# Optimization experiments

Measured on AMD Instinct MI355X. Metric: run time of the kernel, lower is better.

The kernel has to match this reference:

```python
import jax, jax.numpy as jnp
import numpy as np

K = 5
EPS = 1e-08


def setup_inputs() -> dict:
    key = jax.random.key(0)
    x = jax.random.normal(key, (8192, 512), dtype=jnp.float32)
    return {"x": x}


def reference(x):
    n = x.shape[0]
    # torch: everything below through topk is under no_grad, and x is rebound
    # to the normalized tensor, so the whole graph is detached from the input.
    xn = x / jnp.linalg.norm(x, axis=1, keepdims=True)
    xn = jax.lax.stop_gradient(xn)
    dots = xn @ xn.T                                  # [N, N]
    dots = jnp.where(jnp.eye(n, dtype=bool), jnp.float32(-1.0), dots)
    _, topk_idx = jax.lax.top_k(dots, K)              # [N, K]
    x_neighbors = xn[topk_idx]                        # [N, K, D]
    diffs = xn[:, None, :] - x_neighbors              # [N, K, D]
    distances = jnp.linalg.norm(diffs, axis=-1)       # [N, K]
    mean_rho = distances.mean(axis=1)                 # [N]
    loss = -jnp.mean(jnp.log(mean_rho + EPS))
    return loss
```

## Files before the change

kernel.cpp:

```cpp
#include <hip/hip_runtime.h>
#include <math.h>

#define NROWS 8192
#define DIM   512
#define KNN   5
#define EPSV  1e-8f

#define BM 128
#define BN 128
#define BK 32
#define NT (NROWS / BM)
#define NT64 (NROWS / 64)
#define NKS (DIM / BK)
#define NWORK 2080
#define NSEL (NROWS / 4)

typedef __attribute__((ext_vector_type(8))) _Float16 f16x8;
typedef __attribute__((ext_vector_type(4))) float    f32x4;

__device__ __forceinline__ void gload16(const _Float16* g, _Float16* l) {
    __builtin_amdgcn_global_load_lds(
        (const __attribute__((address_space(1))) void*)g,
        (__attribute__((address_space(3))) void*)l, 16, 0, 0);
}

__device__ __forceinline__ void cmpswap(float& a, float& b) {
    const float hi = fmaxf(a, b), lo = fminf(a, b);
    a = hi; b = lo;
}

__device__ __forceinline__ void merge5(float a[KNN], const float b[KNN]) {
    const float c0 = fmaxf(a[0], b[0]);
    const float c1 = fmaxf(fmaxf(a[1], b[1]), fminf(a[0], b[0]));
    const float c2 = fmaxf(fmaxf(a[2], b[2]),
                           fmaxf(fminf(a[0], b[1]), fminf(a[1], b[0])));
    const float c3 = fmaxf(fmaxf(a[3], b[3]),
                           fmaxf(fminf(a[0], b[2]),
                                 fmaxf(fminf(a[1], b[1]), fminf(a[2], b[0]))));
    const float c4 = fmaxf(fmaxf(a[4], b[4]),
                           fmaxf(fmaxf(fminf(a[0], b[3]), fminf(a[1], b[2])),
                                 fmaxf(fminf(a[2], b[1]), fminf(a[3], b[0]))));
    a[0] = c0; a[1] = c1; a[2] = c2; a[3] = c3; a[4] = c4;
}

__global__ __launch_bounds__(256) void norm_kernel(const float* __restrict__ x,
                                                   _Float16* __restrict__ xnh) {
    const int wv = threadIdx.x >> 6, lane = threadIdx.x & 63;
    const int row = blockIdx.x * 4 + wv;
    const float4* xr = (const float4*)(x + (size_t)row * DIM) + lane * 2;
    const float4 a = xr[0];
    const float4 b = xr[1];
    float s = a.x * a.x + a.y * a.y + a.z * a.z + a.w * a.w
            + b.x * b.x + b.y * b.y + b.z * b.z + b.w * b.w;
    #pragma unroll
    for (int off = 1; off < 64; off <<= 1) s += __shfl_xor(s, off, 64);
    const float inv = 1.0f / sqrtf(s);
    const f16x8 h = { (_Float16)(a.x * inv), (_Float16)(a.y * inv),
                      (_Float16)(a.z * inv), (_Float16)(a.w * inv),
                      (_Float16)(b.x * inv), (_Float16)(b.y * inv),
                      (_Float16)(b.z * inv), (_Float16)(b.w * inv) };
    *(f16x8*)(xnh + (size_t)row * DIM + lane * 8) = h;
}

__global__ __launch_bounds__(256) void dots_top3_kernel(const _Float16* __restrict__ xnh,
                                                        float* __restrict__ M3) {
    int I, J;
    {
        int rem = (int)(blockIdx.x & 7) * (NWORK / 8) + (int)(blockIdx.x >> 3);
        int found = 0;
        for (int SI = 0; SI < 8 && !found; ++SI) {
            for (int SJ = SI; SJ < 8 && !found; ++SJ) {
                const int sz = (SI == SJ) ? 36 : 64;
                if (rem < sz) {
                    if (SI == SJ) {
                        int i = 0, r2 = rem;
                        while (r2 >= 8 - i) { r2 -= 8 - i; ++i; }
                        I = SI * 8 + i;
                        J = SJ * 8 + i + r2;
                    } else {
                        I = SI * 8 + (rem >> 3);
                        J = SJ * 8 + (rem & 7);
                    }
                    found = 1;
                } else {
                    rem -= sz;
                }
            }
        }
    }

    __shared__ __align__(16) _Float16 As[BM * BK];
    __shared__ __align__(16) _Float16 Bs[BN * BK];

    const int tid    = threadIdx.x;
    const int lane   = tid & 63;
    const int wv     = tid >> 6;
    const int wm     = wv >> 1;
    const int wn     = wv & 1;
    const int m_lane = lane & 15;
    const int quad   = lane >> 4;

    const int i0 = I * BM;
    const int j0 = J * BN;

    const int rowlocal = (m_lane >> 2) * 16 + quad * 4 + (m_lane & 3);
    const int myrow    = i0 + wm * 64 + rowlocal;

    const int rchunk = (quad ^ ((m_lane >> 1) & 3)) * 8;

    f32x4 acc[4][4];
    #pragma unroll
    for (int m = 0; m < 4; ++m)
        #pragma unroll
        for (int n = 0; n < 4; ++n)
            acc[m][n] = (f32x4){0.f, 0.f, 0.f, 0.f};

    for (int ks = 0; ks < NKS; ++ks) {
        const int k0 = ks * BK;
        #pragma unroll
        for (int q = 0; q < 2; ++q) {
            const int s  = tid + q * 256;
            const int r  = s >> 2;
            const int kg = (s & 3) ^ ((s >> 3) & 3);
            gload16(xnh + (size_t)(i0 + r) * DIM + k0 + kg * 8, As + s * 8);
            gload16(xnh + (size_t)(j0 + r) * DIM + k0 + kg * 8, Bs + s * 8);
        }
        __syncthreads();

        f16x8 af[4], bf[4];
        #pragma unroll
        for (int m = 0; m < 4; ++m)
            af[m] = *(const f16x8*)(As + (wm * 64 + m * 16 + m_lane) * BK + rchunk);
        #pragma unroll
        for (int n = 0; n < 4; ++n)
            bf[n] = *(const f16x8*)(Bs + (wn * 64 + n * 16 + m_lane) * BK + rchunk);
        #pragma unroll
        for (int m = 0; m < 4; ++m)
            #pragma unroll
            for (int n = 0; n < 4; ++n)
                acc[m][n] = __builtin_amdgcn_mfma_f32_16x16x32_f16(af[m], bf[n], acc[m][n], 0, 0, 0);
        __syncthreads();
    }

    const bool diag = (I == J) && (wm == wn);
    #pragma unroll
    for (int m = 0; m < 4; ++m)
        #pragma unroll
        for (int i = 0; i < 4; ++i)
            acc[m][m][i] = (diag && (quad * 4 + i) == m_lane) ? -2.f : acc[m][m][i];

    float g1 = -2.f, g2 = -2.f, g3 = -2.f;
    #pragma unroll
    for (int m = 0; m < 4; ++m) {
        #pragma unroll
        for (int i = 0; i < 4; ++i) {
            float v0 = acc[m][0][i], v1 = acc[m][1][i];
            float v2 = acc[m][2][i], v3 = acc[m][3][i];
            cmpswap(v0, v1); cmpswap(v2, v3);
            cmpswap(v0, v2); cmpswap(v1, v3);
            cmpswap(v1, v2);
            float a1 = v0, a2 = v1, a3 = v2;
            #pragma unroll
            for (int d = 1; d < 16; d <<= 1) {
                const float b1 = __shfl_xor(a1, d, 64);
                const float b2 = __shfl_xor(a2, d, 64);
                const float b3 = __shfl_xor(a3, d, 64);
                const float n1 = fmaxf(a1, b1);
                const float n2 = fmaxf(fminf(a1, b1), fmaxf(a2, b2));
                const float n3 = fmaxf(fmaxf(a3, b3),
                                       fmaxf(fminf(a1, b2), fminf(a2, b1)));
                a1 = n1; a2 = n2; a3 = n3;
            }
            const bool own = (m_lane == m * 4 + i);
            g1 = own ? a1 : g1; g2 = own ? a2 : g2; g3 = own ? a3 : g3;
        }
    }
    {
        float* p = M3 + ((size_t)myrow * NT64 + (J * 2 + wn)) * 3;
        p[0] = g1; p[1] = g2; p[2] = g3;
    }

    if (I != J) {
        #pragma unroll
        for (int n = 0; n < 4; ++n) {
            float c1 = -2.f, c2 = -2.f, c3 = -2.f;
            #pragma unroll
            for (int m = 0; m < 4; ++m)
                #pragma unroll
                for (int i = 0; i < 4; ++i) {
                    const float v  = acc[m][n][i];
                    const float u1 = fminf(c1, v);
                    c1 = fmaxf(c1, v);
                    const float u2 = fminf(c2, u1);
                    c2 = fmaxf(c2, u1);
                    c3 = fmaxf(c3, u2);
                }
            #pragma unroll
            for (int d = 16; d < 64; d <<= 1) {
                const float b1 = __shfl_xor(c1, d, 64);
                const float b2 = __shfl_xor(c2, d, 64);
                const float b3 = __shfl_xor(c3, d, 64);
                const float n2 = fmaxf(fminf(c1, b1), fmaxf(c2, b2));
                const float n3 = fmaxf(fmaxf(c3, b3),
                                       fmaxf(fminf(c1, b2), fminf(c2, b1)));
                c1 = fmaxf(c1, b1); c2 = n2; c3 = n3;
            }
            if (quad == 0) {
                const int col = j0 + wn * 64 + n * 16 + m_lane;
                float* p = M3 + ((size_t)col * NT64 + (I * 2 + wm)) * 3;
                p[0] = c1; p[1] = c2; p[2] = c3;
            }
        }
    }
}

__global__ __launch_bounds__(256) void select_loss_kernel(const _Float16* __restrict__ xnh,
                                                          const float* __restrict__ M3,
                                                          float* __restrict__ partials) {
    const int wv = threadIdx.x >> 6, lane = threadIdx.x & 63;
    const int row = blockIdx.x * 4 + wv;
    const float* p = M3 + (size_t)row * NT64 * 3 + lane * 6;
    float a[3], b[3];
    a[0] = p[0]; a[1] = p[1]; a[2] = p[2];
    b[0] = p[3]; b[1] = p[4]; b[2] = p[5];

    float t[KNN];
    {
        float c[KNN] = { a[0], a[1], a[2], -2.f, -2.f };
        const float bb[KNN] = { b[0], b[1], b[2], -2.f, -2.f };
        merge5(c, bb);
        #pragma unroll
        for (int d = 1; d < 64; d <<= 1) {
            float o[KNN];
            #pragma unroll
            for (int k = 0; k < KNN; ++k) o[k] = __shfl_xor(c[k], d, 64);
            merge5(c, o);
        }
        #pragma unroll
        for (int k = 0; k < KNN; ++k) t[k] = c[k];
    }

    const unsigned long long ba = __ballot(a[2] >= t[4]);
    const unsigned long long bb_ = __ballot(b[2] >= t[4]);
    if (ba | bb_) {
        const bool fA = (ba >> lane) & 1ull, fB = (bb_ >> lane) & 1ull;
        float c[KNN] = { fA ? -2.f : a[0], fA ? -2.f : a[1], fA ? -2.f : a[2],
                         -2.f, -2.f };
        const float b5[KNN] = { fB ? -2.f : b[0], fB ? -2.f : b[1],
                                fB ? -2.f : b[2], -2.f, -2.f };
        merge5(c, b5);
        #pragma unroll
        for (int d = 1; d < 64; d <<= 1) {
            float o[KNN];
            #pragma unroll
            for (int k = 0; k < KNN; ++k) o[k] = __shfl_xor(c[k], d, 64);
            merge5(c, o);
        }
        #pragma unroll
        for (int k = 0; k < KNN; ++k) t[k] = c[k];

        unsigned long long fl[2] = { ba, bb_ };
        #pragma unroll
        for (int h = 0; h < 2; ++h) {
            unsigned long long m = fl[h];
            while (m) {
                const int l = __ffsll((long long)m) - 1;
                m &= m - 1;
                const int jt2 = 2 * l + h;
                const int col = jt2 * 64 + lane;
                const _Float16* rp = xnh + (size_t)row * DIM;
                const _Float16* cp = xnh + (size_t)col * DIM;
                float d = 0.f;
                for (int k8 = 0; k8 < DIM / 8; ++k8) {
                    const f16x8 rv = *(const f16x8*)(rp + k8 * 8);
                    const f16x8 cv = *(const f16x8*)(cp + k8 * 8);
                    #pragma unroll
                    for (int e = 0; e < 8; ++e)
                        d += (float)rv[e] * (float)cv[e];
                }
                if (col == row) d = -2.f;
                float c2[KNN] = { d, -2.f, -2.f, -2.f, -2.f };
                #pragma unroll
                for (int dd = 1; dd < 64; dd <<= 1) {
                    float o[KNN];
                    #pragma unroll
                    for (int k = 0; k < KNN; ++k) o[k] = __shfl_xor(c2[k], dd, 64);
                    merge5(c2, o);
                }
                merge5(t, c2);
            }
        }
    }

    float s = 0.f;
    #pragma unroll
    for (int k = 0; k < KNN; ++k) s += sqrtf(fmaxf(2.f - 2.f * t[k], 0.f));
    const float val = logf(s * (1.f / KNN) + EPSV);

    __shared__ float red[4];
    if (lane == 0) red[wv] = val;
    __syncthreads();
    if (threadIdx.x == 0)
        partials[blockIdx.x] = red[0] + red[1] + red[2] + red[3];
}

__global__ __launch_bounds__(256) void reduce_kernel(const float* __restrict__ partials,
                                                     float* __restrict__ out) {
    const int tid = threadIdx.x, lane = tid & 63, wv = tid >> 6;
    float s = 0.f;
    #pragma unroll
    for (int q = 0; q < NSEL / 256; ++q) s += partials[tid + q * 256];
    #pragma unroll
    for (int off = 1; off < 64; off <<= 1) s += __shfl_xor(s, off, 64);
    __shared__ float red[4];
    if (lane == 0) red[wv] = s;
    __syncthreads();
    if (tid == 0)
        *out = -(red[0] + red[1] + red[2] + red[3]) / (float)NROWS;
}

extern "C" void kernel_launch(void* const* d_in, const int* in_sizes, int n_in,
                              void* d_out, int out_size, void* d_ws, size_t ws_size,
                              hipStream_t stream) {
    const float* x = (const float*)d_in[0];
    float* out = (float*)d_out;
    char* ws = (char*)d_ws;

    _Float16* xnh = (_Float16*)ws;
    float* M3 = (float*)(ws + (size_t)NROWS * DIM * sizeof(_Float16));
    float* partials = M3 + (size_t)NROWS * NT64 * 3;

    norm_kernel<<<NROWS / 4, 256, 0, stream>>>(x, xnh);
    dots_top3_kernel<<<NWORK, 256, 0, stream>>>(xnh, M3);
    select_loss_kernel<<<NSEL, 256, 0, stream>>>(xnh, M3, partials);
    reduce_kernel<<<1, 256, 0, stream>>>(partials, out);
}
```

Measured before the change: 144.7 us.

## Split dots tile across eight waves with LDS merge of column top-3

The symmetric dot-product tile kernel now runs 512 threads (8 waves) per 128x128 tile instead of 4. Each wave computes a 32x64 sub-tile, which halves per-wave accumulators and gives each wave a single staging load per k-step. Column top-3 partials from wave pairs are merged through LDS before being written. The aim is more latency hiding and occupancy, at the cost of an extra barrier, LDS traffic and less MFMA work per wave.

```diff
diff --git a/kernel.cpp b/kernel.cpp
--- a/kernel.cpp
+++ b/kernel.cpp
@@ -62,7 +62,7 @@
     *(f16x8*)(xnh + (size_t)row * DIM + lane * 8) = h;
 }
 
-__global__ __launch_bounds__(256) void dots_top3_kernel(const _Float16* __restrict__ xnh,
+__global__ __launch_bounds__(512) void dots_top3_kernel(const _Float16* __restrict__ xnh,
                                                         float* __restrict__ M3) {
     int I, J;
     {
@@ -103,23 +103,19 @@
     const int i0 = I * BM;
     const int j0 = J * BN;
 
-    const int rowlocal = (m_lane >> 2) * 16 + quad * 4 + (m_lane & 3);
-    const int myrow    = i0 + wm * 64 + rowlocal;
-
     const int rchunk = (quad ^ ((m_lane >> 1) & 3)) * 8;
 
-    f32x4 acc[4][4];
-    #pragma unroll
-    for (int m = 0; m < 4; ++m)
+    f32x4 acc[2][4];
+    #pragma unroll
+    for (int m = 0; m < 2; ++m)
         #pragma unroll
         for (int n = 0; n < 4; ++n)
             acc[m][n] = (f32x4){0.f, 0.f, 0.f, 0.f};
 
     for (int ks = 0; ks < NKS; ++ks) {
         const int k0 = ks * BK;
-        #pragma unroll
-        for (int q = 0; q < 2; ++q) {
-            const int s  = tid + q * 256;
+        {
+            const int s  = tid;
             const int r  = s >> 2;
             const int kg = (s & 3) ^ ((s >> 3) & 3);
             gload16(xnh + (size_t)(i0 + r) * DIM + k0 + kg * 8, As + s * 8);
@@ -127,31 +123,36 @@
         }
         __syncthreads();
 
-        f16x8 af[4], bf[4];
-        #pragma unroll
-        for (int m = 0; m < 4; ++m)
-            af[m] = *(const f16x8*)(As + (wm * 64 + m * 16 + m_lane) * BK + rchunk);
+        f16x8 af[2], bf[4];
+        #pragma unroll
+        for (int m = 0; m < 2; ++m)
+            af[m] = *(const f16x8*)(As + (wm * 32 + m * 16 + m_lane) * BK + rchunk);
         #pragma unroll
         for (int n = 0; n < 4; ++n)
             bf[n] = *(const f16x8*)(Bs + (wn * 64 + n * 16 + m_lane) * BK + rchunk);
         #pragma unroll
-        for (int m = 0; m < 4; ++m)
+        for (int m = 0; m < 2; ++m)
             #pragma unroll
             for (int n = 0; n < 4; ++n)
                 acc[m][n] = __builtin_amdgcn_mfma_f32_16x16x32_f16(af[m], bf[n], acc[m][n], 0, 0, 0);
         __syncthreads();
     }
 
-    const bool diag = (I == J) && (wm == wn);
-    #pragma unroll
-    for (int m = 0; m < 4; ++m)
-        #pragma unroll
-        for (int i = 0; i < 4; ++i)
-            acc[m][m][i] = (diag && (quad * 4 + i) == m_lane) ? -2.f : acc[m][m][i];
+    if (I == J) {
+        #pragma unroll
+        for (int m = 0; m < 2; ++m)
+            #pragma unroll
+            for (int n = 0; n < 4; ++n)
+                if ((2 * wm + m) == (4 * wn + n)) {
+                    #pragma unroll
+                    for (int i = 0; i < 4; ++i)
+                        acc[m][n][i] = ((quad * 4 + i) == m_lane) ? -2.f : acc[m][n][i];
+                }
+    }
 
     float g1 = -2.f, g2 = -2.f, g3 = -2.f;
     #pragma unroll
-    for (int m = 0; m < 4; ++m) {
+    for (int m = 0; m < 2; ++m) {
         #pragma unroll
         for (int i = 0; i < 4; ++i) {
             float v0 = acc[m][0][i], v1 = acc[m][1][i];
@@ -175,17 +176,20 @@
             g1 = own ? a1 : g1; g2 = own ? a2 : g2; g3 = own ? a3 : g3;
         }
     }
-    {
+    if (m_lane < 8) {
+        const int rowlocal = (m_lane >> 2) * 16 + quad * 4 + (m_lane & 3);
+        const int myrow    = i0 + wm * 32 + rowlocal;
         float* p = M3 + ((size_t)myrow * NT64 + (J * 2 + wn)) * 3;
         p[0] = g1; p[1] = g2; p[2] = g3;
     }
 
     if (I != J) {
+        float* cb = (float*)As;
         #pragma unroll
         for (int n = 0; n < 4; ++n) {
             float c1 = -2.f, c2 = -2.f, c3 = -2.f;
             #pragma unroll
-            for (int m = 0; m < 4; ++m)
+            for (int m = 0; m < 2; ++m)
                 #pragma unroll
                 for (int i = 0; i < 4; ++i) {
                     const float v  = acc[m][n][i];
@@ -206,10 +210,23 @@
                 c1 = fmaxf(c1, b1); c2 = n2; c3 = n3;
             }
             if (quad == 0) {
-                const int col = j0 + wn * 64 + n * 16 + m_lane;
-                float* p = M3 + ((size_t)col * NT64 + (I * 2 + wm)) * 3;
-                p[0] = c1; p[1] = c2; p[2] = c3;
-            }
+                const int idx = (wv * 64 + n * 16 + m_lane) * 3;
+                cb[idx + 0] = c1; cb[idx + 1] = c2; cb[idx + 2] = c3;
+            }
+        }
+        __syncthreads();
+        if (!(wm & 1)) {
+            const int me = (wv * 64 + lane) * 3;
+            const int pr = (((wm + 1) * 2 + wn) * 64 + lane) * 3;
+            const float a1 = cb[me], a2 = cb[me + 1], a3 = cb[me + 2];
+            const float b1 = cb[pr], b2 = cb[pr + 1], b3 = cb[pr + 2];
+            const float n1 = fmaxf(a1, b1);
+            const float n2 = fmaxf(fminf(a1, b1), fmaxf(a2, b2));
+            const float n3 = fmaxf(fmaxf(a3, b3),
+                                   fmaxf(fminf(a1, b2), fminf(a2, b1)));
+            const int col = j0 + wn * 64 + lane;
+            float* p = M3 + ((size_t)col * NT64 + (I * 2 + (wm >> 1))) * 3;
+            p[0] = n1; p[1] = n2; p[2] = n3;
         }
     }
 }
@@ -331,7 +348,7 @@
     float* partials = M3 + (size_t)NROWS * NT64 * 3;
 
     norm_kernel<<<NROWS / 4, 256, 0, stream>>>(x, xnh);
-    dots_top3_kernel<<<NWORK, 256, 0, stream>>>(xnh, M3);
+    dots_top3_kernel<<<NWORK, 512, 0, stream>>>(xnh, M3);
     select_loss_kernel<<<NSEL, 256, 0, stream>>>(xnh, M3, partials);
     reduce_kernel<<<1, 256, 0, stream>>>(partials, out);
 }
```

Result: slower. 159.5 us (+10.2%).
